# Optimization experiments

Hardware: AMD Instinct MI355X
Metric: run time of the kernel (lower is better)

## Reference

```python
import jax, jax.numpy as jnp
import numpy as np

H = 16  # num_heads


def setup_inputs() -> dict:
    key = jax.random.key(0)
    ks = jax.random.split(key, 7)
    S, HID, D = 8192, 1280, 80
    n_chunks = 8
    x = jax.random.normal(ks[0], (S, HID), dtype=jnp.float32)
    cos = jax.random.uniform(ks[1], (S, D), dtype=jnp.float32)
    sin = jax.random.uniform(ks[2], (S, D), dtype=jnp.float32)
    Wqkv = jax.random.normal(ks[3], (HID, 3 * HID), dtype=jnp.float32) * (HID ** -0.5)
    bqkv = jnp.zeros((3 * HID,), dtype=jnp.float32)
    Wproj = jax.random.normal(ks[4], (HID, HID), dtype=jnp.float32) * (HID ** -0.5)
    bproj = jnp.zeros((HID,), dtype=jnp.float32)
    cu_seqlens = (jnp.arange(n_chunks + 1, dtype=jnp.int32) * (S // n_chunks))
    return {"x": x, "cos": cos, "sin": sin, "Wqkv": Wqkv, "bqkv": bqkv,
            "Wproj": Wproj, "bproj": bproj, "cu_seqlens": cu_seqlens}


def _apply_rotary(t, cos, sin):
    # t: (S, H, D); cos/sin: (S, D)
    d2 = t.shape[-1] // 2
    x1, x2 = t[..., :d2], t[..., d2:]
    rotated = jnp.concatenate([-x2, x1], axis=-1)
    return t * cos[:, None, :] + rotated * sin[:, None, :]


def reference(x, cos, sin, Wqkv, bqkv, Wproj, bproj, cu_seqlens):
    S, HID = x.shape
    D = HID // H
    inv_scale = 1.0 / np.sqrt(D)
    qkv = (x @ Wqkv + bqkv).reshape(S, 3, H, D)
    q, k, v = qkv[:, 0], qkv[:, 1], qkv[:, 2]  # each (S, H, D)
    q = _apply_rotary(q, cos, sin)
    k = _apply_rotary(k, cos, sin)
    # Equal-size windows: reshape to (n_chunks, L, H, D) -> block-diagonal attention.
    C = cu_seqlens.shape[0] - 1
    L = S // C
    qc = q.reshape(C, L, H, D)
    kc = k.reshape(C, L, H, D)
    vc = v.reshape(C, L, H, D)
    scores = jnp.einsum('cihd,cjhd->chij', qc, kc) * inv_scale
    probs = jax.nn.softmax(scores.astype(jnp.float32), axis=-1).astype(x.dtype)
    out = jnp.einsum('chij,cjhd->cihd', probs, vc)  # (C, L, H, D)
    out = out.reshape(S, HID)
    return out @ Wproj + bproj
```

## Files before the change

### kernel.cpp

```cpp
#include <hip/hip_runtime.h>
#include <math.h>
#include <stdint.h>

#define S_LEN 8192
#define HID   1280
#define NH    16
#define HD    80
#define LCH   1024
#define NCH   8

typedef __attribute__((ext_vector_type(8))) short bf16x8;
typedef __attribute__((ext_vector_type(8))) unsigned short u16x8;
typedef __attribute__((ext_vector_type(4))) float f32x4;

__device__ __forceinline__ uint16_t f2bf(float f) {
    union { float f; uint32_t u; } v; v.f = f;
    uint32_t r = v.u + 0x7FFF + ((v.u >> 16) & 1);
    return (uint16_t)(r >> 16);
}
__device__ __forceinline__ float bf2f(uint16_t h) {
    union { uint32_t u; float f; } v; v.u = ((uint32_t)h) << 16;
    return v.f;
}
__device__ __forceinline__ uint32_t pk2(float a, float b) {
    union { float f; uint32_t u; } x, y; x.f = a; y.f = b;
    return (x.u >> 16) | (y.u & 0xFFFF0000u);
}

__device__ __forceinline__ void glds16(const void* g, void* l) {
    __builtin_amdgcn_global_load_lds(
        (const __attribute__((address_space(1))) uint32_t*)g,
        (__attribute__((address_space(3))) uint32_t*)l,
        16, 0, 0);
}

#define MFMA16(a, b, c) __builtin_amdgcn_mfma_f32_16x16x32_bf16(a, b, c, 0, 0, 0)
#define SB()  __builtin_amdgcn_sched_barrier(0)
#define BAR() __builtin_amdgcn_s_barrier()

template<int N> __device__ __forceinline__ void vmwait() {
    if constexpr (N == 0) asm volatile("s_waitcnt vmcnt(0)" ::: "memory");
    else if constexpr (N == 2) asm volatile("s_waitcnt vmcnt(2)" ::: "memory");
    else if constexpr (N == 4) asm volatile("s_waitcnt vmcnt(4)" ::: "memory");
}

__device__ __forceinline__ void stage_tile(const char* gsrc, char* dst, int w,
                                           int kt, int nbytes)
{
    const char* sp = gsrc + (size_t)kt * 64;
    int off = w * 1024;
    glds16(sp + (size_t)off * 40, dst + off);
    off += 8192;
    if (off < nbytes) glds16(sp + (size_t)off * 40, dst + off);
}

__global__ __launch_bounds__(256)
void xsplit_kernel(const float* __restrict__ x, uint16_t* __restrict__ xh,
                   uint16_t* __restrict__ xl)
{
    int idx = (blockIdx.x * 256 + threadIdx.x) * 4;
    float4 v = *(const float4*)(x + idx);
    ushort4 hi, lo;
    hi.x = f2bf(v.x); lo.x = f2bf(v.x - bf2f(hi.x));
    hi.y = f2bf(v.y); lo.y = f2bf(v.y - bf2f(hi.y));
    hi.z = f2bf(v.z); lo.z = f2bf(v.z - bf2f(hi.z));
    hi.w = f2bf(v.w); lo.w = f2bf(v.w - bf2f(hi.w));
    *(ushort4*)(xh + idx) = hi;
    *(ushort4*)(xl + idx) = lo;
}

template<int ND>
__global__ __launch_bounds__(256)
void wsplit_kernel(const float* __restrict__ W, uint16_t* __restrict__ Wth,
                   uint16_t* __restrict__ Wtl)
{
    __shared__ float t[32][33];
    const int tid = threadIdx.x;
    const int n0 = blockIdx.x * 32;
    const int k0 = blockIdx.y * 32;
    for (int i = tid; i < 1024; i += 256) {
        int r = i >> 5, c = i & 31;
        t[r][c] = W[(size_t)(k0 + r) * ND + n0 + c];
    }
    __syncthreads();
    for (int i = tid; i < 1024; i += 256) {
        int r = i >> 5, c = i & 31;
        float f = t[c][r];
        uint16_t hi = f2bf(f);
        size_t o = (size_t)(n0 + r) * HID + k0 + c;
        Wth[o] = hi;
        Wtl[o] = f2bf(f - bf2f(hi));
    }
}

template<int BM, int ND, int BN, int NWM, int NWN, int EPI, int W1>
__global__ __launch_bounds__(512, 2)
void gemm8p(const uint16_t* __restrict__ Ahp, const uint16_t* __restrict__ Alp,
            const uint16_t* __restrict__ Bth, const uint16_t* __restrict__ Btl,
            const float* __restrict__ bias, float* __restrict__ oF,
            uint16_t* __restrict__ oq, uint16_t* __restrict__ ok,
            uint16_t* __restrict__ ov)
{
    constexpr int MI  = BM / (NWM * 16);
    constexpr int NI  = BN / (NWN * 16);
    constexpr int ABYTES = BM * 64;
    constexpr int BBYTES = BN * 64;
    constexpr int NT = HID / 32;
    static_assert(NWM * NWN == 8, "8 waves");
    static_assert(BM % (NWM * 16) == 0 && BN % (NWN * 16) == 0, "tile split");

    __shared__ __align__(1024) uint16_t AsH[2][ABYTES / 2];
    __shared__ __align__(1024) uint16_t AsL[2][ABYTES / 2];
    __shared__ __align__(1024) uint16_t BsH[2][BBYTES / 2];
    __shared__ __align__(1024) uint16_t BsL[2][BBYTES / 2];

    const int tid  = threadIdx.x;
    const int w    = tid >> 6;
    const int lane = tid & 63;
    const int quad = lane >> 4;
    const int l16  = lane & 15;
    const int wm   = w / NWN;
    const int wn   = w % NWN;

    const int n0 = blockIdx.x * BN;
    const int m0 = blockIdx.y * BM;

    const size_t stg = (size_t)(lane >> 2) * (HID * 2)
                     + (size_t)(((lane & 3) ^ ((lane >> 3) & 3)) << 4);
    const char* gAh = (const char*)Ahp + (size_t)m0 * (HID * 2) + stg;
    const char* gAl = (const char*)Alp + (size_t)m0 * (HID * 2) + stg;
    const char* gBh = (const char*)Bth + (size_t)n0 * (HID * 2) + stg;
    const char* gBl = (const char*)Btl + (size_t)n0 * (HID * 2) + stg;

    const int swz  = (quad ^ ((l16 >> 1) & 3)) << 4;
    const int aoff = (wm * (MI * 16) + l16) * 64 + swz;
    const int boff = (wn * (NI * 16) + l16) * 64 + swz;

    f32x4 acc[MI][NI];
    #pragma unroll
    for (int mi = 0; mi < MI; ++mi)
        #pragma unroll
        for (int ni = 0; ni < NI; ++ni) acc[mi][ni] = (f32x4){0.f, 0.f, 0.f, 0.f};

    stage_tile(gAh, (char*)AsH[0], w, 0, ABYTES);
    stage_tile(gBh, (char*)BsH[0], w, 0, BBYTES);
    stage_tile(gBl, (char*)BsL[0], w, 0, BBYTES);
    stage_tile(gAl, (char*)AsL[0], w, 0, ABYTES);
    SB(); vmwait<W1>(); BAR(); SB();

    for (int kt = 0; kt < NT - 1; ++kt) {
        const int s = kt & 1, t = s ^ 1;
        bf16x8 ah[MI], bh[NI];

        #pragma unroll
        for (int mi = 0; mi < MI; ++mi)
            ah[mi] = *(const bf16x8*)((const char*)AsH[s] + aoff + mi * 1024);
        #pragma unroll
        for (int ni = 0; ni < NI; ++ni)
            bh[ni] = *(const bf16x8*)((const char*)BsH[s] + boff + ni * 1024);
        stage_tile(gAh, (char*)AsH[t], w, kt + 1, ABYTES);
        stage_tile(gBh, (char*)BsH[t], w, kt + 1, BBYTES);
        SB(); vmwait<W1>(); BAR(); SB();
        __builtin_amdgcn_s_setprio(1);
        #pragma unroll
        for (int mi = 0; mi < MI; ++mi)
            #pragma unroll
            for (int ni = 0; ni < NI; ++ni)
                acc[mi][ni] = MFMA16(ah[mi], bh[ni], acc[mi][ni]);
        __builtin_amdgcn_s_setprio(0);

        bf16x8 bl[NI];
        #pragma unroll
        for (int ni = 0; ni < NI; ++ni)
            bl[ni] = *(const bf16x8*)((const char*)BsL[s] + boff + ni * 1024);
        stage_tile(gBl, (char*)BsL[t], w, kt + 1, BBYTES);
        stage_tile(gAl, (char*)AsL[t], w, kt + 1, ABYTES);
        SB(); BAR(); SB();
        __builtin_amdgcn_s_setprio(1);
        #pragma unroll
        for (int mi = 0; mi < MI; ++mi)
            #pragma unroll
            for (int ni = 0; ni < NI; ++ni)
                acc[mi][ni] = MFMA16(ah[mi], bl[ni], acc[mi][ni]);
        __builtin_amdgcn_s_setprio(0);

        bf16x8 al[MI];
        #pragma unroll
        for (int mi = 0; mi < MI; ++mi)
            al[mi] = *(const bf16x8*)((const char*)AsL[s] + aoff + mi * 1024);
        SB(); vmwait<W1>(); BAR(); SB();
        __builtin_amdgcn_s_setprio(1);
        #pragma unroll
        for (int mi = 0; mi < MI; ++mi)
            #pragma unroll
            for (int ni = 0; ni < NI; ++ni)
                acc[mi][ni] = MFMA16(al[mi], bh[ni], acc[mi][ni]);
        __builtin_amdgcn_s_setprio(0);
    }

    {
        const int s = (NT - 1) & 1;
        bf16x8 ah[MI], bh[NI];
        #pragma unroll
        for (int mi = 0; mi < MI; ++mi)
            ah[mi] = *(const bf16x8*)((const char*)AsH[s] + aoff + mi * 1024);
        #pragma unroll
        for (int ni = 0; ni < NI; ++ni)
            bh[ni] = *(const bf16x8*)((const char*)BsH[s] + boff + ni * 1024);
        SB(); vmwait<0>(); BAR(); SB();
        __builtin_amdgcn_s_setprio(1);
        #pragma unroll
        for (int mi = 0; mi < MI; ++mi)
            #pragma unroll
            for (int ni = 0; ni < NI; ++ni)
                acc[mi][ni] = MFMA16(ah[mi], bh[ni], acc[mi][ni]);
        __builtin_amdgcn_s_setprio(0);

        bf16x8 bl[NI];
        #pragma unroll
        for (int ni = 0; ni < NI; ++ni)
            bl[ni] = *(const bf16x8*)((const char*)BsL[s] + boff + ni * 1024);
        #pragma unroll
        for (int mi = 0; mi < MI; ++mi)
            #pragma unroll
            for (int ni = 0; ni < NI; ++ni)
                acc[mi][ni] = MFMA16(ah[mi], bl[ni], acc[mi][ni]);

        bf16x8 al[MI];
        #pragma unroll
        for (int mi = 0; mi < MI; ++mi)
            al[mi] = *(const bf16x8*)((const char*)AsL[s] + aoff + mi * 1024);
        #pragma unroll
        for (int mi = 0; mi < MI; ++mi)
            #pragma unroll
            for (int ni = 0; ni < NI; ++ni)
                acc[mi][ni] = MFMA16(al[mi], bh[ni], acc[mi][ni]);
    }

    #pragma unroll
    for (int ni = 0; ni < NI; ++ni) {
        const int n = n0 + wn * (NI * 16) + ni * 16 + l16;
        const float bv = bias[n];
        if constexpr (EPI) {
            const int tq  = n / HID;
            const int rem = n - tq * HID;
            const int h   = rem / HD;
            const int d   = rem - h * HD;
            #pragma unroll
            for (int mi = 0; mi < MI; ++mi) {
                const int mb = m0 + wm * (MI * 16) + mi * 16 + quad * 4;
                if (tq == 2) {
                    ushort4 pv;
                    pv.x = f2bf(acc[mi][ni][0] + bv);
                    pv.y = f2bf(acc[mi][ni][1] + bv);
                    pv.z = f2bf(acc[mi][ni][2] + bv);
                    pv.w = f2bf(acc[mi][ni][3] + bv);
                    *(ushort4*)&ov[((size_t)h * HD + d) * S_LEN + mb] = pv;
                } else {
                    uint16_t* dst = (tq == 0) ? oq : ok;
                    #pragma unroll
                    for (int r = 0; r < 4; ++r)
                        dst[((size_t)h * S_LEN + (mb + r)) * HD + d] =
                            f2bf(acc[mi][ni][r] + bv);
                }
            }
        } else {
            #pragma unroll
            for (int mi = 0; mi < MI; ++mi) {
                const int mb = m0 + wm * (MI * 16) + mi * 16 + quad * 4;
                #pragma unroll
                for (int r = 0; r < 4; ++r)
                    oF[(size_t)(mb + r) * ND + n] = acc[mi][ni][r] + bv;
            }
        }
    }
}

__global__ __launch_bounds__(256)
void rope_kernel(uint16_t* __restrict__ qb, uint16_t* __restrict__ kb,
                 const float* __restrict__ cosb, const float* __restrict__ sinb)
{
    const int t = blockIdx.x * 256 + threadIdx.x;
    const int s = t & (S_LEN - 1);
    uint16_t* qr = qb + (size_t)t * HD;
    uint16_t* kr = kb + (size_t)t * HD;
    const float* cr = cosb + (size_t)s * HD;
    const float* sr = sinb + (size_t)s * HD;
    #pragma unroll
    for (int ch = 0; ch < 5; ++ch) {
        const int d = ch * 8;
        u16x8 q1 = *(const u16x8*)(qr + d);
        u16x8 q2 = *(const u16x8*)(qr + d + 40);
        u16x8 k1 = *(const u16x8*)(kr + d);
        u16x8 k2 = *(const u16x8*)(kr + d + 40);
        float c1[8], c2[8], s1[8], s2[8];
        *(float4*)&c1[0] = *(const float4*)(cr + d);
        *(float4*)&c1[4] = *(const float4*)(cr + d + 4);
        *(float4*)&c2[0] = *(const float4*)(cr + d + 40);
        *(float4*)&c2[4] = *(const float4*)(cr + d + 44);
        *(float4*)&s1[0] = *(const float4*)(sr + d);
        *(float4*)&s1[4] = *(const float4*)(sr + d + 4);
        *(float4*)&s2[0] = *(const float4*)(sr + d + 40);
        *(float4*)&s2[4] = *(const float4*)(sr + d + 44);
        u16x8 o1, o2, p1, p2;
        #pragma unroll
        for (int j = 0; j < 8; ++j) {
            float q1f = bf2f((uint16_t)q1[j]), q2f = bf2f((uint16_t)q2[j]);
            o1[j] = f2bf(q1f * c1[j] - q2f * s1[j]);
            o2[j] = f2bf(q2f * c2[j] + q1f * s2[j]);
            float k1f = bf2f((uint16_t)k1[j]), k2f = bf2f((uint16_t)k2[j]);
            p1[j] = f2bf(k1f * c1[j] - k2f * s1[j]);
            p2[j] = f2bf(k2f * c2[j] + k1f * s2[j]);
        }
        *(u16x8*)(qr + d)      = o1;
        *(u16x8*)(qr + d + 40) = o2;
        *(u16x8*)(kr + d)      = p1;
        *(u16x8*)(kr + d + 40) = p2;
    }
}

#define BQ 256
#define BK 64

__device__ __forceinline__ void kstage(const char* kg, char* dst, int w, int lane)
{
    int p = w * 1024 + lane * 16;
    {
        int row = p >> 7;
        int sl  = (p >> 4) & 7;
        glds16(kg + row * 160 + ((sl ^ (row & 7)) << 4), dst + p);
    }
    int p2 = p + 8192;
    if (p2 < 10240) {
        int q   = p2 - 8192;
        int row = q >> 5;
        int sl  = (q >> 4) & 1;
        glds16(kg + row * 160 + 128 + (sl << 4), dst + p2);
    }
}

__global__ __launch_bounds__(512, 4)
void attn_kernel(const uint16_t* __restrict__ qb, const uint16_t* __restrict__ kb,
                 const uint16_t* __restrict__ vt,
                 uint16_t* __restrict__ abh, uint16_t* __restrict__ abl)
{
    __shared__ __align__(16) uint16_t smemA[BQ * HD];
    __shared__ __align__(16) uint16_t ksm[2][BK * HD];
    __shared__ __align__(16) uint16_t vsm[HD * BK];

    const int tid  = threadIdx.x;
    const int w    = tid >> 6;
    const int lane = tid & 63;
    const int quad = lane >> 4;
    const int l16  = lane & 15;

    const int qt = blockIdx.x;
    const int h  = blockIdx.y;
    const int c  = blockIdx.z;
    const int q0 = c * LCH + qt * BQ;

    uint16_t (*psw)[68] = (uint16_t(*)[68])smemA + w * 32;

    {
        const char* qg = (const char*)(qb + ((size_t)h * S_LEN + q0) * HD);
        for (int off = w * 1024; off < BQ * HD * 2; off += 8192)
            glds16(qg + off + lane * 16, (char*)smemA + off);
    }
    __syncthreads();

    bf16x8 qfr[2][3];
    #pragma unroll
    for (int mi = 0; mi < 2; ++mi) {
        const int row = w * 32 + mi * 16 + l16;
        qfr[mi][0] = *(const bf16x8*)&smemA[row * HD + quad * 8];
        qfr[mi][1] = *(const bf16x8*)&smemA[row * HD + 32 + quad * 8];
        bf16x8 z = {0, 0, 0, 0, 0, 0, 0, 0};
        qfr[mi][2] = (quad < 2) ? *(const bf16x8*)&smemA[row * HD + 64 + quad * 8] : z;
    }

    bf16x8 vf5;
    {
        short o = (l16 == 0) ? (short)0x3F80 : (short)0;
        vf5 = (bf16x8){o, o, o, o, o, o, o, o};
    }

    f32x4 Oacc[2][6];
    #pragma unroll
    for (int mi = 0; mi < 2; ++mi)
        #pragma unroll
        for (int d = 0; d < 6; d++) Oacc[mi][d] = (f32x4){0.f, 0.f, 0.f, 0.f};

    const float C2 = 0.11180339887498949f * 1.4426950408889634f;
    const char* kg0 = (const char*)(kb + ((size_t)h * S_LEN + c * LCH) * HD);
    const size_t vrow_stride = (size_t)S_LEN * 2;
    const char* vg0 = (const char*)vt + (size_t)h * HD * S_LEN * 2 + (size_t)(c * LCH) * 2;

    kstage(kg0, (char*)&ksm[0][0], w, lane);

    for (int kt = 0; kt < LCH / BK; ++kt) {
        __syncthreads();

        {
            const char* vg = vg0 + (size_t)(kt * BK) * 2;
            for (int off = w * 1024; off < HD * BK * 2; off += 8192) {
                int o   = off + lane * 16;
                int row = o >> 7;
                int col = o & 127;
                glds16(vg + (size_t)row * vrow_stride + (col ^ ((row & 7) << 4)),
                       (char*)vsm + off);
            }
        }

        const char* ksb = (const char*)&ksm[kt & 1][0];
        #pragma unroll
        for (int ns = 0; ns < 4; ++ns) {
            const int kr = ns * 16 + l16;
            const int sw = (kr & 7) << 4;
            bf16x8 kf0 = *(const bf16x8*)(ksb + kr * 128 + ((quad * 16) ^ sw));
            bf16x8 kf1 = *(const bf16x8*)(ksb + kr * 128 + ((64 + quad * 16) ^ sw));
            bf16x8 z = {0, 0, 0, 0, 0, 0, 0, 0};
            bf16x8 kf2 = (quad < 2)
                ? *(const bf16x8*)(ksb + 8192 + kr * 32 + quad * 16) : z;
            #pragma unroll
            for (int mi = 0; mi < 2; ++mi) {
                f32x4 s = (f32x4){0.f, 0.f, 0.f, 0.f};
                s = MFMA16(kf0, qfr[mi][0], s);
                s = MFMA16(kf1, qfr[mi][1], s);
                s = MFMA16(kf2, qfr[mi][2], s);
                float e0 = exp2f(s[0] * C2);
                float e1 = exp2f(s[1] * C2);
                float e2 = exp2f(s[2] * C2);
                float e3 = exp2f(s[3] * C2);
                *(uint2*)&psw[mi * 16 + l16][ns * 16 + quad * 4] =
                    (uint2){pk2(e0, e1), pk2(e2, e3)};
            }
        }

        __syncthreads();

        if (kt + 1 < LCH / BK)
            kstage(kg0 + (size_t)(kt + 1) * BK * HD * 2,
                   (char*)&ksm[(kt + 1) & 1][0], w, lane);

        #pragma unroll
        for (int kc = 0; kc < 2; ++kc) {
            bf16x8 pf[2];
            #pragma unroll
            for (int mi = 0; mi < 2; ++mi) {
                const uint16_t* pp = &psw[mi * 16 + l16][kc * 32 + quad * 8];
                ((uint2*)&pf[mi])[0] = *(const uint2*)(pp);
                ((uint2*)&pf[mi])[1] = *(const uint2*)(pp + 4);
            }
            #pragma unroll
            for (int ds = 0; ds < 5; ++ds) {
                const int vr = ds * 16 + l16;
                bf16x8 vf = *(const bf16x8*)((const char*)vsm + vr * 128 +
                    ((kc * 64 + quad * 16) ^ ((vr & 7) << 4)));
                #pragma unroll
                for (int mi = 0; mi < 2; ++mi)
                    Oacc[mi][ds] = MFMA16(pf[mi], vf, Oacc[mi][ds]);
            }
            #pragma unroll
            for (int mi = 0; mi < 2; ++mi)
                Oacc[mi][5] = MFMA16(pf[mi], vf5, Oacc[mi][5]);
        }
    }

    #pragma unroll
    for (int mi = 0; mi < 2; ++mi)
        #pragma unroll
        for (int r = 0; r < 4; ++r) {
            float l = __shfl(Oacc[mi][5][r], lane & 48);
            float inv = 1.f / l;
            const int srow = q0 + w * 32 + mi * 16 + quad * 4 + r;
            const size_t rowbase = (size_t)srow * HID + h * HD;
            #pragma unroll
            for (int ds = 0; ds < 5; ++ds) {
                float f = Oacc[mi][ds][r] * inv;
                uint16_t hi = f2bf(f);
                abh[rowbase + ds * 16 + l16] = hi;
                abl[rowbase + ds * 16 + l16] = f2bf(f - bf2f(hi));
            }
        }
}

extern "C" void kernel_launch(void* const* d_in, const int* in_sizes, int n_in,
                              void* d_out, int out_size, void* d_ws, size_t ws_size,
                              hipStream_t stream)
{
    const float* x     = (const float*)d_in[0];
    const float* cosb  = (const float*)d_in[1];
    const float* sinb  = (const float*)d_in[2];
    const float* Wqkv  = (const float*)d_in[3];
    const float* bqkv  = (const float*)d_in[4];
    const float* Wproj = (const float*)d_in[5];
    const float* bproj = (const float*)d_in[6];
    float* out = (float*)d_out;

    const size_t E = (size_t)NH * S_LEN * HD;
    uint16_t* qb  = (uint16_t*)d_ws;
    uint16_t* kb  = qb + E;
    uint16_t* vt  = kb + E;
    uint16_t* xh  = vt + E;
    uint16_t* xl  = xh + E;
    uint16_t* wth = xl + E;
    uint16_t* wtl = wth + (size_t)3 * HID * HID;

    xsplit_kernel<<<(S_LEN * HID) / (256 * 4), 256, 0, stream>>>(x, xh, xl);
    wsplit_kernel<3 * HID><<<dim3(3 * HID / 32, HID / 32), 256, 0, stream>>>(Wqkv, wth, wtl);
    gemm8p<256, 3 * HID, 256, 2, 4, 1, 4>
        <<<dim3(3 * HID / 256, S_LEN / 256), 512, 0, stream>>>(
        xh, xl, wth, wtl, bqkv, nullptr, qb, kb, vt);
    rope_kernel<<<(NH * S_LEN) / 256, 256, 0, stream>>>(qb, kb, cosb, sinb);
    attn_kernel<<<dim3(LCH / BQ, NH, NCH), 512, 0, stream>>>(qb, kb, vt, xh, xl);
    wsplit_kernel<HID><<<dim3(HID / 32, HID / 32), 256, 0, stream>>>(Wproj, wth, wtl);
    gemm8p<128, HID, 160, 4, 2, 0, 2>
        <<<dim3(HID / 160, S_LEN / 128), 512, 0, stream>>>(
        xh, xl, wth, wtl, bproj, out, nullptr, nullptr, nullptr);
}
```

Measured before the change: 525.0 us.

## Double-buffer V tiles in attention, drop mid-loop barrier, enlarge projection GEMM tile

The attention kernel now keeps two V buffers in shared memory. The next K and V tiles are prefetched right after the loop-top barrier, so the second __syncthreads per iteration is gone and the loads overlap with the QK and PV MFMA work. This costs extra shared memory, which could hurt occupancy. Separately, the output projection GEMM uses a 256-row tile with a deeper pipeline parameter (3), which needed a new vmcnt(3) wait variant.

After: 524.6 us. No clear change (-0.1%).

```diff
diff --git a/kernel.cpp b/kernel.cpp
--- a/kernel.cpp
+++ b/kernel.cpp
@@ -41,6 +41,7 @@
 template<int N> __device__ __forceinline__ void vmwait() {
     if constexpr (N == 0) asm volatile("s_waitcnt vmcnt(0)" ::: "memory");
     else if constexpr (N == 2) asm volatile("s_waitcnt vmcnt(2)" ::: "memory");
+    else if constexpr (N == 3) asm volatile("s_waitcnt vmcnt(3)" ::: "memory");
     else if constexpr (N == 4) asm volatile("s_waitcnt vmcnt(4)" ::: "memory");
 }
 
@@ -339,6 +340,17 @@
     }
 }
 
+__device__ __forceinline__ void vstage(const char* vg, char* dst, size_t vrow_stride,
+                                       int w, int lane)
+{
+    for (int off = w * 1024; off < HD * BK * 2; off += 8192) {
+        int o   = off + lane * 16;
+        int row = o >> 7;
+        int col = o & 127;
+        glds16(vg + (size_t)row * vrow_stride + (col ^ ((row & 7) << 4)), dst + off);
+    }
+}
+
 __global__ __launch_bounds__(512, 4)
 void attn_kernel(const uint16_t* __restrict__ qb, const uint16_t* __restrict__ kb,
                  const uint16_t* __restrict__ vt,
@@ -346,7 +358,7 @@
 {
     __shared__ __align__(16) uint16_t smemA[BQ * HD];
     __shared__ __align__(16) uint16_t ksm[2][BK * HD];
-    __shared__ __align__(16) uint16_t vsm[HD * BK];
+    __shared__ __align__(16) uint16_t vsm[2][HD * BK];
 
     const int tid  = threadIdx.x;
     const int w    = tid >> 6;
@@ -396,22 +408,20 @@
     const char* vg0 = (const char*)vt + (size_t)h * HD * S_LEN * 2 + (size_t)(c * LCH) * 2;
 
     kstage(kg0, (char*)&ksm[0][0], w, lane);
+    vstage(vg0, (char*)&vsm[0][0], vrow_stride, w, lane);
 
     for (int kt = 0; kt < LCH / BK; ++kt) {
+        const int s = kt & 1;
         __syncthreads();
 
-        {
-            const char* vg = vg0 + (size_t)(kt * BK) * 2;
-            for (int off = w * 1024; off < HD * BK * 2; off += 8192) {
-                int o   = off + lane * 16;
-                int row = o >> 7;
-                int col = o & 127;
-                glds16(vg + (size_t)row * vrow_stride + (col ^ ((row & 7) << 4)),
-                       (char*)vsm + off);
-            }
+        if (kt + 1 < LCH / BK) {
+            kstage(kg0 + (size_t)(kt + 1) * BK * HD * 2,
+                   (char*)&ksm[s ^ 1][0], w, lane);
+            vstage(vg0 + (size_t)((kt + 1) * BK) * 2,
+                   (char*)&vsm[s ^ 1][0], vrow_stride, w, lane);
         }
 
-        const char* ksb = (const char*)&ksm[kt & 1][0];
+        const char* ksb = (const char*)&ksm[s][0];
         #pragma unroll
         for (int ns = 0; ns < 4; ++ns) {
             const int kr = ns * 16 + l16;
@@ -423,25 +433,20 @@
                 ? *(const bf16x8*)(ksb + 8192 + kr * 32 + quad * 16) : z;
             #pragma unroll
             for (int mi = 0; mi < 2; ++mi) {
-                f32x4 s = (f32x4){0.f, 0.f, 0.f, 0.f};
-                s = MFMA16(kf0, qfr[mi][0], s);
-                s = MFMA16(kf1, qfr[mi][1], s);
-                s = MFMA16(kf2, qfr[mi][2], s);
-                float e0 = exp2f(s[0] * C2);
-                float e1 = exp2f(s[1] * C2);
-                float e2 = exp2f(s[2] * C2);
-                float e3 = exp2f(s[3] * C2);
+                f32x4 sv = (f32x4){0.f, 0.f, 0.f, 0.f};
+                sv = MFMA16(kf0, qfr[mi][0], sv);
+                sv = MFMA16(kf1, qfr[mi][1], sv);
+                sv = MFMA16(kf2, qfr[mi][2], sv);
+                float e0 = exp2f(sv[0] * C2);
+                float e1 = exp2f(sv[1] * C2);
+                float e2 = exp2f(sv[2] * C2);
+                float e3 = exp2f(sv[3] * C2);
                 *(uint2*)&psw[mi * 16 + l16][ns * 16 + quad * 4] =
                     (uint2){pk2(e0, e1), pk2(e2, e3)};
             }
         }
 
-        __syncthreads();
-
-        if (kt + 1 < LCH / BK)
-            kstage(kg0 + (size_t)(kt + 1) * BK * HD * 2,
-                   (char*)&ksm[(kt + 1) & 1][0], w, lane);
-
+        const char* vsb = (const char*)&vsm[s][0];
         #pragma unroll
         for (int kc = 0; kc < 2; ++kc) {
             bf16x8 pf[2];
@@ -454,7 +459,7 @@
             #pragma unroll
             for (int ds = 0; ds < 5; ++ds) {
                 const int vr = ds * 16 + l16;
-                bf16x8 vf = *(const bf16x8*)((const char*)vsm + vr * 128 +
+                bf16x8 vf = *(const bf16x8*)(vsb + vr * 128 +
                     ((kc * 64 + quad * 16) ^ ((vr & 7) << 4)));
                 #pragma unroll
                 for (int mi = 0; mi < 2; ++mi)
@@ -514,7 +519,7 @@
     rope_kernel<<<(NH * S_LEN) / 256, 256, 0, stream>>>(qb, kb, cosb, sinb);
     attn_kernel<<<dim3(LCH / BQ, NH, NCH), 512, 0, stream>>>(qb, kb, vt, xh, xl);
     wsplit_kernel<HID><<<dim3(HID / 32, HID / 32), 256, 0, stream>>>(Wproj, wth, wtl);
-    gemm8p<128, HID, 160, 4, 2, 0, 2>
-        <<<dim3(HID / 160, S_LEN / 128), 512, 0, stream>>>(
+    gemm8p<256, HID, 160, 4, 2, 0, 3>
+        <<<dim3(HID / 160, S_LEN / 256), 512, 0, stream>>>(
         xh, xl, wth, wtl, bproj, out, nullptr, nullptr, nullptr);
 }
```
